# Optimization experiments

Hardware: AMD Instinct MI355X
Metric: run time of the kernel (lower is better)

Reference implementation:

```python
import jax, jax.numpy as jnp
import numpy as np

INNER_D = 4096
LORA_RANK = 2
LORA_ALPHA = 1.0
BATCH, SEQ = 4, 4096


def setup_inputs() -> dict:
    key = jax.random.key(0)
    k_x, k_aq, k_bq, k_as, k_bs = jax.random.split(key, 5)
    x_in = jax.random.normal(k_x, (BATCH, SEQ, INNER_D), dtype=jnp.float32)
    # bnb int8 quantized LoRA weights (row-major [out, in], as nn.Linear stores)
    a_q = jax.random.randint(k_aq, (LORA_RANK, INNER_D), -127, 128, dtype=jnp.int8)
    b_q = jax.random.randint(k_bq, (INNER_D, LORA_RANK), -127, 128, dtype=jnp.int8)
    # per-output-row dequant scales (absmax/127), small positive values
    a_scale = jax.random.uniform(k_as, (LORA_RANK,), jnp.float32, 0.005, 0.02)
    b_scale = jax.random.uniform(k_bs, (INNER_D,), jnp.float32, 0.005, 0.02)
    return {"x_in": x_in, "a_q": a_q, "a_scale": a_scale, "b_q": b_q, "b_scale": b_scale}


def reference(x_in, a_q, a_scale, b_q, b_scale):
    scale = LORA_ALPHA / LORA_RANK  # lora_alpha / lora_rank = 0.5
    # inline dequantization: int8 weight * per-row scale
    A = a_q.astype(jnp.float32) * a_scale[:, None]   # [rank, d]
    B = b_q.astype(jnp.float32) * b_scale[:, None]   # [d, rank]
    h = jnp.einsum('bsd,rd->bsr', x_in, A)           # lora_a(x)
    out = scale * jnp.einsum('bsr,dr->bsd', h, B)    # (alpha/rank) * lora_b(h)
    return out
```

## Files before the change

kernel.cpp:

```cpp
#include <hip/hip_runtime.h>
#include <hip/hip_bf16.h>


#define QL_D 4096
#define QL_ROWS 16384

__global__ __launch_bounds__(256) void qlora_fused_kernel(
    const float* __restrict__ x,
    const int*   __restrict__ a_q,
    const float* __restrict__ a_scale,
    const int*   __restrict__ b_q,
    const float* __restrict__ b_scale,
    float*       __restrict__ out)
{
    const int row = blockIdx.x;
    const int t   = threadIdx.x;

    const float* xr   = x   + (size_t)row * QL_D;
    float*       outr = out + (size_t)row * QL_D;

    float h0 = 0.0f, h1 = 0.0f;
    const float4* xr4 = (const float4*)xr;
    const int4*   a0p = (const int4*)a_q;
    const int4*   a1p = (const int4*)(a_q + QL_D);

#pragma unroll
    for (int k = 0; k < 4; ++k) {
        const int d4 = t + 256 * k;
        const float4 xv = xr4[d4];
        const int4   a0 = a0p[d4];
        const int4   a1 = a1p[d4];
        h0 += xv.x * (float)a0.x + xv.y * (float)a0.y
            + xv.z * (float)a0.z + xv.w * (float)a0.w;
        h1 += xv.x * (float)a1.x + xv.y * (float)a1.y
            + xv.z * (float)a1.z + xv.w * (float)a1.w;
    }

#pragma unroll
    for (int off = 32; off > 0; off >>= 1) {
        h0 += __shfl_down(h0, off, 64);
        h1 += __shfl_down(h1, off, 64);
    }

    __shared__ float s0[4], s1[4];
    const int wave = t >> 6;
    const int lane = t & 63;
    if (lane == 0) { s0[wave] = h0; s1[wave] = h1; }
    __syncthreads();

    const float H0 = (s0[0] + s0[1] + s0[2] + s0[3]) * a_scale[0];
    const float H1 = (s1[0] + s1[1] + s1[2] + s1[3]) * a_scale[1];

    const int4*   bq4 = (const int4*)b_q;
    const float4* bs4 = (const float4*)b_scale;

#pragma unroll
    for (int k = 0; k < 4; ++k) {
        const int d4 = t + 256 * k;
        const float4 bs  = bs4[d4];
        const int4   bq0 = bq4[2 * d4];
        const int4   bq1 = bq4[2 * d4 + 1];
        float4 o;
        o.x = 0.5f * bs.x * (H0 * (float)bq0.x + H1 * (float)bq0.y);
        o.y = 0.5f * bs.y * (H0 * (float)bq0.z + H1 * (float)bq0.w);
        o.z = 0.5f * bs.z * (H0 * (float)bq1.x + H1 * (float)bq1.y);
        o.w = 0.5f * bs.w * (H0 * (float)bq1.z + H1 * (float)bq1.w);
        ((float4*)outr)[d4] = o;
    }
}

extern "C" void kernel_launch(void* const* d_in, const int* in_sizes, int n_in,
                              void* d_out, int out_size, void* d_ws, size_t ws_size,
                              hipStream_t stream) {
    const float* x       = (const float*)d_in[0];
    const int*   a_q     = (const int*)d_in[1];
    const float* a_scale = (const float*)d_in[2];
    const int*   b_q     = (const int*)d_in[3];
    const float* b_scale = (const float*)d_in[4];
    float*       out     = (float*)d_out;

    qlora_fused_kernel<<<QL_ROWS, 256, 0, stream>>>(x, a_q, a_scale, b_q, b_scale, out);
}
```

Measured before the change: 451.5 us.

## Split fused LoRA kernel into two multi-row kernels with register-cached weights

```diff
diff --git a/kernel.cpp b/kernel.cpp
--- a/kernel.cpp
+++ b/kernel.cpp
@@ -2,70 +2,104 @@
 #include <hip/hip_bf16.h>
 
 
-#define QL_D 4096
+#define QL_D    4096
 #define QL_ROWS 16384
+#define K1_ROWS 4
+#define K2_ROWS 8
 
-__global__ __launch_bounds__(256) void qlora_fused_kernel(
+__global__ __launch_bounds__(256) void qlora_h_kernel(
     const float* __restrict__ x,
     const int*   __restrict__ a_q,
     const float* __restrict__ a_scale,
-    const int*   __restrict__ b_q,
-    const float* __restrict__ b_scale,
-    float*       __restrict__ out)
+    float2*      __restrict__ h_out)
 {
-    const int row = blockIdx.x;
-    const int t   = threadIdx.x;
+    const int t    = threadIdx.x;
+    const int row0 = blockIdx.x * K1_ROWS;
 
-    const float* xr   = x   + (size_t)row * QL_D;
-    float*       outr = out + (size_t)row * QL_D;
+    float fa0[16], fa1[16];
+    const int4* a0p = (const int4*)a_q;
+    const int4* a1p = (const int4*)(a_q + QL_D);
+#pragma unroll
+    for (int k = 0; k < 4; ++k) {
+        const int4 q0 = a0p[t + 256 * k];
+        const int4 q1 = a1p[t + 256 * k];
+        fa0[4*k+0] = (float)q0.x; fa0[4*k+1] = (float)q0.y;
+        fa0[4*k+2] = (float)q0.z; fa0[4*k+3] = (float)q0.w;
+        fa1[4*k+0] = (float)q1.x; fa1[4*k+1] = (float)q1.y;
+        fa1[4*k+2] = (float)q1.z; fa1[4*k+3] = (float)q1.w;
+    }
 
-    float h0 = 0.0f, h1 = 0.0f;
-    const float4* xr4 = (const float4*)xr;
-    const int4*   a0p = (const int4*)a_q;
-    const int4*   a1p = (const int4*)(a_q + QL_D);
+    __shared__ float s0[K1_ROWS][4], s1[K1_ROWS][4];
+    const int wave = t >> 6;
+    const int lane = t & 63;
 
+    const float4* x4 = (const float4*)(x + (size_t)row0 * QL_D);
+
+#pragma unroll
+    for (int r = 0; r < K1_ROWS; ++r) {
+        float h0 = 0.0f, h1 = 0.0f;
+#pragma unroll
+        for (int k = 0; k < 4; ++k) {
+            const float4 xv = x4[r * (QL_D / 4) + t + 256 * k];
+            h0 += xv.x * fa0[4*k+0] + xv.y * fa0[4*k+1]
+                + xv.z * fa0[4*k+2] + xv.w * fa0[4*k+3];
+            h1 += xv.x * fa1[4*k+0] + xv.y * fa1[4*k+1]
+                + xv.z * fa1[4*k+2] + xv.w * fa1[4*k+3];
+        }
+#pragma unroll
+        for (int off = 32; off > 0; off >>= 1) {
+            h0 += __shfl_down(h0, off, 64);
+            h1 += __shfl_down(h1, off, 64);
+        }
+        if (lane == 0) { s0[r][wave] = h0; s1[r][wave] = h1; }
+    }
+    __syncthreads();
+
+    if (t < K1_ROWS) {
+        const float H0 = (s0[t][0] + s0[t][1] + s0[t][2] + s0[t][3]) * a_scale[0];
+        const float H1 = (s1[t][0] + s1[t][1] + s1[t][2] + s1[t][3]) * a_scale[1];
+        h_out[row0 + t] = make_float2(H0, H1);
+    }
+}
+
+__global__ __launch_bounds__(256) void qlora_out_kernel(
+    const float2* __restrict__ h_in,
+    const int*    __restrict__ b_q,
+    const float*  __restrict__ b_scale,
+    float*        __restrict__ out)
+{
+    const int t    = threadIdx.x;
+    const int row0 = blockIdx.x * K2_ROWS;
+
+    float bb0[16], bb1[16];
+    const int4*   bq4 = (const int4*)b_q;
+    const float4* bs4 = (const float4*)b_scale;
 #pragma unroll
     for (int k = 0; k < 4; ++k) {
         const int d4 = t + 256 * k;
-        const float4 xv = xr4[d4];
-        const int4   a0 = a0p[d4];
-        const int4   a1 = a1p[d4];
-        h0 += xv.x * (float)a0.x + xv.y * (float)a0.y
-            + xv.z * (float)a0.z + xv.w * (float)a0.w;
-        h1 += xv.x * (float)a1.x + xv.y * (float)a1.y
-            + xv.z * (float)a1.z + xv.w * (float)a1.w;
+        const float4 bs = bs4[d4];
+        const int4   q0 = bq4[2 * d4];
+        const int4   q1 = bq4[2 * d4 + 1];
+        bb0[4*k+0] = 0.5f * bs.x * (float)q0.x; bb1[4*k+0] = 0.5f * bs.x * (float)q0.y;
+        bb0[4*k+1] = 0.5f * bs.y * (float)q0.z; bb1[4*k+1] = 0.5f * bs.y * (float)q0.w;
+        bb0[4*k+2] = 0.5f * bs.z * (float)q1.x; bb1[4*k+2] = 0.5f * bs.z * (float)q1.y;
+        bb0[4*k+3] = 0.5f * bs.w * (float)q1.z; bb1[4*k+3] = 0.5f * bs.w * (float)q1.w;
     }
 
+    float4* o4 = (float4*)(out + (size_t)row0 * QL_D);
+
+#pragma unroll 2
+    for (int r = 0; r < K2_ROWS; ++r) {
+        const float2 h = h_in[row0 + r];
 #pragma unroll
-    for (int off = 32; off > 0; off >>= 1) {
-        h0 += __shfl_down(h0, off, 64);
-        h1 += __shfl_down(h1, off, 64);
-    }
-
-    __shared__ float s0[4], s1[4];
-    const int wave = t >> 6;
-    const int lane = t & 63;
-    if (lane == 0) { s0[wave] = h0; s1[wave] = h1; }
-    __syncthreads();
-
-    const float H0 = (s0[0] + s0[1] + s0[2] + s0[3]) * a_scale[0];
-    const float H1 = (s1[0] + s1[1] + s1[2] + s1[3]) * a_scale[1];
-
-    const int4*   bq4 = (const int4*)b_q;
-    const float4* bs4 = (const float4*)b_scale;
-
-#pragma unroll
-    for (int k = 0; k < 4; ++k) {
-        const int d4 = t + 256 * k;
-        const float4 bs  = bs4[d4];
-        const int4   bq0 = bq4[2 * d4];
-        const int4   bq1 = bq4[2 * d4 + 1];
-        float4 o;
-        o.x = 0.5f * bs.x * (H0 * (float)bq0.x + H1 * (float)bq0.y);
-        o.y = 0.5f * bs.y * (H0 * (float)bq0.z + H1 * (float)bq0.w);
-        o.z = 0.5f * bs.z * (H0 * (float)bq1.x + H1 * (float)bq1.y);
-        o.w = 0.5f * bs.w * (H0 * (float)bq1.z + H1 * (float)bq1.w);
-        ((float4*)outr)[d4] = o;
+        for (int k = 0; k < 4; ++k) {
+            float4 o;
+            o.x = h.x * bb0[4*k+0] + h.y * bb1[4*k+0];
+            o.y = h.x * bb0[4*k+1] + h.y * bb1[4*k+1];
+            o.z = h.x * bb0[4*k+2] + h.y * bb1[4*k+2];
+            o.w = h.x * bb0[4*k+3] + h.y * bb1[4*k+3];
+            o4[r * (QL_D / 4) + t + 256 * k] = o;
+        }
     }
 }
 
@@ -78,6 +112,8 @@
     const int*   b_q     = (const int*)d_in[3];
     const float* b_scale = (const float*)d_in[4];
     float*       out     = (float*)d_out;
+    float2*      h_ws    = (float2*)d_ws;
 
-    qlora_fused_kernel<<<QL_ROWS, 256, 0, stream>>>(x, a_q, a_scale, b_q, b_scale, out);
+    qlora_h_kernel  <<<QL_ROWS / K1_ROWS, 256, 0, stream>>>(x, a_q, a_scale, h_ws);
+    qlora_out_kernel<<<QL_ROWS / K2_ROWS, 256, 0, stream>>>(h_ws, b_q, b_scale, out);
 }
```

Measured after the change: 451.1 us. Within noise of the previous version (-0.1%).
